# Optimization experiments

Measured on AMD Instinct MI355X. Metric: run time of the kernel, lower is better.

The kernel has to match this reference:

```python
import jax, jax.numpy as jnp
import numpy as np

NUM_BINS = 512
NUM_HEADS = 8
CHANNELS = 512
FFN_HIDDEN = 1024
BN_EPS = 1e-5


def setup_inputs() -> dict:
    key = jax.random.key(0)
    ks = jax.random.split(key, 8)
    B, C, N = 32, CHANNELS, 512
    Fh = FFN_HIDDEN
    inp = {
        "x": jax.random.normal(ks[0], (B, C, N), dtype=jnp.float32),
        "qkv_w": jax.random.normal(ks[1], (3 * C, C), dtype=jnp.float32) * 0.02,
        "qkv_b": jnp.zeros((3 * C,), jnp.float32),
        "out_w": jax.random.normal(ks[2], (C, C), dtype=jnp.float32) * 0.02,
        "out_b": jnp.zeros((C,), jnp.float32),
        "rel_pos_emb": jax.random.normal(ks[3], (2 * NUM_BINS - 1, NUM_HEADS), dtype=jnp.float32) * 0.02,
        "bn1_g": jnp.ones((C,), jnp.float32),
        "bn1_b": jnp.zeros((C,), jnp.float32),
        "bn1_m": jnp.zeros((C,), jnp.float32),
        "bn1_v": jnp.ones((C,), jnp.float32),
        "ffn1_w": jax.random.normal(ks[4], (Fh, C), dtype=jnp.float32) * 0.02,
        "ffn1_b": jnp.zeros((Fh,), jnp.float32),
        "ffn2_w": jax.random.normal(ks[5], (C, Fh), dtype=jnp.float32) * 0.02,
        "ffn2_b": jnp.zeros((C,), jnp.float32),
        "bn2_g": jnp.ones((C,), jnp.float32),
        "bn2_b": jnp.zeros((C,), jnp.float32),
        "bn2_m": jnp.zeros((C,), jnp.float32),
        "bn2_v": jnp.ones((C,), jnp.float32),
    }
    return inp


def _pw_conv(w, b, x):
    # 1x1 Conv1d == per-position linear: w [O, C], x [B, C, N] -> [B, O, N]
    return jnp.einsum('oc,bcn->bon', w, x) + b[None, :, None]


def _bn_eval(x, g, b, m, v):
    # BatchNorm1d in eval mode over channel dim of [B, C, N]
    inv = jax.lax.rsqrt(v + BN_EPS)
    return (x - m[None, :, None]) * (g * inv)[None, :, None] + b[None, :, None]


def reference(x, qkv_w, qkv_b, out_w, out_b, rel_pos_emb,
              bn1_g, bn1_b, bn1_m, bn1_v,
              ffn1_w, ffn1_b, ffn2_w, ffn2_b,
              bn2_g, bn2_b, bn2_m, bn2_v):
    B, C, N = x.shape
    H = NUM_HEADS
    Dh = C // H
    scale = Dh ** (-0.5)

    residual = x
    qkv = _pw_conv(qkv_w, qkv_b, x)                      # [B, 3C, N]
    q, k, v = jnp.split(qkv, 3, axis=1)
    # view(B, H, Dh, N).transpose(-1, -2) -> [B, H, N, Dh]
    q = jnp.swapaxes(q.reshape(B, H, Dh, N), -1, -2)
    k = jnp.swapaxes(k.reshape(B, H, Dh, N), -1, -2)
    v = jnp.swapaxes(v.reshape(B, H, Dh, N), -1, -2)

    attn = jnp.einsum('bhnd,bhmd->bhnm', q, k) * scale   # [B, H, N, N]

    # relative position bias, gathered from the table
    pos_idx = jnp.arange(N)[None, :] - jnp.arange(N)[:, None]
    pos_idx = jnp.clip(pos_idx + NUM_BINS - 1, 0, 2 * NUM_BINS - 2)
    bias = rel_pos_emb[pos_idx]                          # [N, N, H]
    attn = attn + jnp.transpose(bias, (2, 0, 1))[None]   # [1, H, N, N]

    attn = jax.nn.softmax(attn, axis=-1)
    out = jnp.einsum('bhnm,bhmd->bhnd', attn, v)         # [B, H, N, Dh]
    out = jnp.swapaxes(out, -1, -2).reshape(B, C, N)
    out = _pw_conv(out_w, out_b, out)

    h = _bn_eval(out + residual, bn1_g, bn1_b, bn1_m, bn1_v)

    f = _pw_conv(ffn1_w, ffn1_b, h)
    f = jax.nn.gelu(f, approximate=False)
    f = _pw_conv(ffn2_w, ffn2_b, f)

    return _bn_eval(f + h, bn2_g, bn2_b, bn2_m, bn2_v)
```

## Files before the change

kernel.cpp:

```cpp
#include <hip/hip_runtime.h>
#include <cstddef>
#include <cstdint>

constexpr int B_ = 32;
constexpr int C_ = 512;
constexpr int N_ = 512;
constexpr int H_ = 8;
constexpr int FH_ = 1024;
constexpr float BN_EPS_ = 1e-5f;
constexpr float LOG2E_ = 1.44269504088896f;

typedef __attribute__((ext_vector_type(8))) short bf16x8;
typedef __attribute__((ext_vector_type(4))) short s16x4;
typedef __attribute__((ext_vector_type(4))) float f32x4;

enum { EPI_QKV = 0, EPI_BN1 = 1, EPI_GELU = 2, EPI_BN2 = 3 };

__device__ inline void gload_lds16(const void* g, void* l) {
    __builtin_amdgcn_global_load_lds(
        (const __attribute__((address_space(1))) void*)g,
        (__attribute__((address_space(3))) void*)l, 16, 0, 0);
}

__device__ inline short f2bf(float f) {
    union { float f; uint32_t u; } v; v.f = f;
    uint32_t r = v.u + 0x7fffu + ((v.u >> 16) & 1u);
    return (short)(r >> 16);
}

__device__ inline float bf2f(short s) {
    union { uint32_t u; float f; } v;
    v.u = ((uint32_t)(uint16_t)s) << 16;
    return v.f;
}

__device__ inline uint32_t cvt_pk_bf16(float lo, float hi) {
    uint32_t r;
    asm("v_cvt_pk_bf16_f32 %0, %1, %2" : "=v"(r) : "v"(lo), "v"(hi));
    return r;
}

__global__ __launch_bounds__(256) void cvt_weights(
    const float* __restrict__ s0, const float* __restrict__ s1,
    const float* __restrict__ s2, const float* __restrict__ s3,
    short* __restrict__ d)
{
    int i = blockIdx.x * 256 + threadIdx.x;
    const float* src;
    int local;
    if (i < 196608)      { src = s0; local = i; }
    else if (i < 262144) { src = s1; local = i - 196608; }
    else if (i < 393216) { src = s2; local = i - 262144; }
    else                 { src = s3; local = i - 393216; }
    f32x4 v = *(const f32x4*)&src[(size_t)local * 4];
    s16x4 o;
    o[0] = f2bf(v[0]); o[1] = f2bf(v[1]); o[2] = f2bf(v[2]); o[3] = f2bf(v[3]);
    *(s16x4*)&d[(size_t)i * 4] = o;
}

__global__ __launch_bounds__(256) void transpose_x(const float* __restrict__ x,
                                                   short* __restrict__ xT)
{
    __shared__ __align__(16) float s[64][65];
    const int b = blockIdx.z, c0 = blockIdx.x * 64, n0 = blockIdx.y * 64;
    const int t = threadIdx.x;
    const float* xb = x + ((size_t)b * C_ + c0) * N_ + n0;
    {
        int nl = t & 63, cl = t >> 6;
#pragma unroll
        for (int i = 0; i < 16; ++i)
            s[cl + i * 4][nl] = xb[(size_t)(cl + i * 4) * N_ + nl];
    }
    __syncthreads();
    short* xTb = xT + ((size_t)b * N_ + n0) * C_ + c0;
    {
        int cl = t & 63, nl = t >> 6;
#pragma unroll
        for (int i = 0; i < 16; ++i)
            xTb[(size_t)(nl + i * 4) * C_ + cl] = f2bf(s[cl][nl + i * 4]);
    }
}

template <int EPI, int KD, int OSTR, int OB, int NB>
__global__ __launch_bounds__(256) void gemm_mfma(
    const short* __restrict__ A, const short* __restrict__ W,
    const float* __restrict__ bias,
    short* __restrict__ Yb, short* __restrict__ Yv, float* __restrict__ Yf,
    const short* __restrict__ resb,
    const float* __restrict__ g, const float* __restrict__ bt,
    const float* __restrict__ mn, const float* __restrict__ vr)
{
    constexpr int NWG = OB * NB * B_;
    constexpr int CPX = NWG / 8;
    const int bid = blockIdx.x;
    const int swz = (bid & 7) * CPX + (bid >> 3);
    const int ob  = swz % OB;
    const int rst = swz / OB;
    const int b   = rst / NB;
    const int o0  = ob * 128;
    const int n0  = (rst % NB) * 128;
    const short* Ab = A + (size_t)b * 512 * KD;

    __shared__ __align__(16) short As[4][128 * 32];
    __shared__ __align__(16) short Bs[4][128 * 32];

    const int t = threadIdx.x;
    const int lane = t & 63, w = t >> 6;
    const int l15 = lane & 15, lg = lane >> 4;
    const int wr = w >> 1, wc = w & 1;

    const f32x4 zero4 = {0.f, 0.f, 0.f, 0.f};
    f32x4 acc[4][4];
#pragma unroll
    for (int i = 0; i < 4; ++i)
#pragma unroll
        for (int j = 0; j < 4; ++j) acc[i][j] = zero4;

    const int r0 = t >> 2;
    const int kb = (((t & 3) ^ ((t >> 3) & 3)) * 8);

    constexpr int Kt = KD / 32;

#define GSTAGE(bufi, kk0)                                                        \
    do {                                                                         \
        gload_lds16(Ab + (size_t)(n0 + r0) * KD + (kk0) + kb,      &As[bufi][w * 512]);        \
        gload_lds16(Ab + (size_t)(n0 + r0 + 64) * KD + (kk0) + kb, &As[bufi][w * 512 + 2048]); \
        gload_lds16(W  + (size_t)(o0 + r0) * KD + (kk0) + kb,      &Bs[bufi][w * 512]);        \
        gload_lds16(W  + (size_t)(o0 + r0 + 64) * KD + (kk0) + kb, &Bs[bufi][w * 512 + 2048]); \
    } while (0)

    GSTAGE(0, 0);
    GSTAGE(1, 32);

    const int rsw = (lg ^ ((l15 >> 1) & 3)) * 8;

    for (int kt = 0; kt < Kt; kt += 4) {
#pragma unroll
        for (int u = 0; u < 4; ++u) {
            const int k = kt + u;
            if (k == Kt - 1) asm volatile("s_waitcnt vmcnt(0)" ::: "memory");
            else             asm volatile("s_waitcnt vmcnt(4)" ::: "memory");
            __builtin_amdgcn_s_barrier();
            __builtin_amdgcn_sched_barrier(0);
            if (k + 2 < Kt) GSTAGE((u + 2) & 3, (k + 2) * 32);

            bf16x8 af[4], bf[4];
#pragma unroll
            for (int mi = 0; mi < 4; ++mi)
                af[mi] = *(const bf16x8*)&As[u][(wr * 64 + mi * 16 + l15) * 32 + rsw];
#pragma unroll
            for (int ni = 0; ni < 4; ++ni)
                bf[ni] = *(const bf16x8*)&Bs[u][(wc * 64 + ni * 16 + l15) * 32 + rsw];
#pragma unroll
            for (int mi = 0; mi < 4; ++mi)
#pragma unroll
                for (int ni = 0; ni < 4; ++ni)
                    acc[mi][ni] = __builtin_amdgcn_mfma_f32_16x16x32_bf16(
                        af[mi], bf[ni], acc[mi][ni], 0, 0, 0);
        }
    }
#undef GSTAGE

#pragma unroll
    for (int mi = 0; mi < 4; ++mi) {
        const int nb2 = n0 + wr * 64 + mi * 16 + lg * 4;
#pragma unroll
        for (int ni = 0; ni < 4; ++ni) {
            const int o = o0 + wc * 64 + ni * 16 + l15;
            const float bv = bias[o];
            f32x4 v = acc[mi][ni];
            if constexpr (EPI == EPI_QKV) {
                if (o0 < 1024) {
#pragma unroll
                    for (int r = 0; r < 4; ++r)
                        Yb[((size_t)b * 512 + nb2 + r) * 1024 + o] = f2bf(v[r] + bv);
                } else {
                    s16x4 pk;
#pragma unroll
                    for (int r = 0; r < 4; ++r) pk[r] = f2bf(v[r] + bv);
                    *(s16x4*)&Yv[((size_t)b * 512 + (o - 1024)) * 512 + nb2] = pk;
                }
            } else if constexpr (EPI == EPI_BN1) {
                const float sc = g[o] * rsqrtf(vr[o] + BN_EPS_);
                const float sh = bt[o] - mn[o] * sc;
#pragma unroll
                for (int r = 0; r < 4; ++r) {
                    float rr = bf2f(resb[((size_t)b * 512 + nb2 + r) * 512 + o]);
                    float val = (v[r] + bv + rr) * sc + sh;
                    Yb[((size_t)b * 512 + nb2 + r) * 512 + o] = f2bf(val);
                }
            } else if constexpr (EPI == EPI_GELU) {
#pragma unroll
                for (int r = 0; r < 4; ++r) {
                    float val = v[r] + bv;
                    val = 0.5f * val * (1.0f + erff(val * 0.70710678118654752f));
                    Yb[((size_t)b * 512 + nb2 + r) * OSTR + o] = f2bf(val);
                }
            } else {
                const float sc = g[o] * rsqrtf(vr[o] + BN_EPS_);
                const float sh = bt[o] - mn[o] * sc;
                f32x4 ov;
#pragma unroll
                for (int r = 0; r < 4; ++r) {
                    float hres = bf2f(resb[((size_t)b * 512 + nb2 + r) * 512 + o]);
                    ov[r] = (v[r] + bv + hres) * sc + sh;
                }
                *(f32x4*)&Yf[((size_t)b * 512 + o) * 512 + nb2] = ov;
            }
        }
    }
}

__global__ __launch_bounds__(512) void attn_mfma(
    const short* __restrict__ qkT, const short* __restrict__ vT,
    const float* __restrict__ rel, short* __restrict__ attnT)
{
    const int id = blockIdx.x;
    const int h  = id & 7;
    const int n0 = ((id >> 3) & 3) * 128;
    const int b  = id >> 5;
    const int t  = threadIdx.x;
    const int lane = t & 63, w = t >> 6;
    const int l15 = lane & 15, lg = lane >> 4;

    __shared__ __align__(16) short Ks[2][64 * 64];
    __shared__ __align__(16) short Vs[2][64 * 64];
    __shared__ __align__(16) short Ps[8 * 16 * 64];
    __shared__ __align__(16) float relh[1024];

    const short* qb = qkT + (size_t)b * 512 * 1024;
    const short* vb = vT + (size_t)b * 512 * 512;

    for (int i = t; i < 1023; i += 512) relh[i] = rel[i * H_ + h] * LOG2E_;

    const int qr = w * 16 + l15;
    const short* qrow = qb + (size_t)(n0 + qr) * 1024 + h * 64;
    bf16x8 aq[2];
    aq[0] = *(const bf16x8*)&qrow[lg * 8];
    aq[1] = *(const bf16x8*)&qrow[32 + lg * 8];

#define KSTAGE(bufi, m0s)                                                        \
    do {                                                                         \
        {                                                                        \
            int fl_ = t * 8;                                                     \
            int r_ = fl_ >> 6;                                                   \
            int blk_ = (fl_ >> 3) & 7;                                           \
            int d_ = ((blk_ ^ (r_ & 7)) << 3);                                   \
            gload_lds16(qb + (size_t)((m0s) + r_) * 1024 + 512 + h * 64 + d_,    \
                        &Ks[bufi][w * 512]);                                     \
        }                                                                        \
        {                                                                        \
            int fl_ = t * 8;                                                     \
            int dr_ = fl_ >> 6;                                                  \
            int blk_ = (fl_ >> 3) & 7;                                           \
            int m_ = ((blk_ ^ (dr_ & 7)) << 3);                                  \
            gload_lds16(vb + (size_t)(h * 64 + dr_) * 512 + (m0s) + m_,          \
                        &Vs[bufi][w * 512]);                                     \
        }                                                                        \
    } while (0)

    KSTAGE(0, 0);
    __syncthreads();

    const f32x4 zero4 = {0.f, 0.f, 0.f, 0.f};
    f32x4 acc_o[4];
#pragma unroll
    for (int dj = 0; dj < 4; ++dj) acc_o[dj] = zero4;

    float rmax = -3e38f, rsum = 0.f;

    const int qglob = n0 + qr;

    int cur = 0;
    for (int tile = 0; tile < 8; ++tile) {
        const int m0 = tile * 64;
        if (tile < 7) KSTAGE(cur ^ 1, m0 + 64);

        f32x4 s4[4];
#pragma unroll
        for (int mi = 0; mi < 4; ++mi) s4[mi] = zero4;
#pragma unroll
        for (int kk = 0; kk < 2; ++kk) {
#pragma unroll
            for (int mi = 0; mi < 4; ++mi) {
                int mr = mi * 16 + l15;
                bf16x8 bk = *(const bf16x8*)&Ks[cur][mr * 64 + (((kk * 4 + lg) ^ (mr & 7)) << 3)];
                s4[mi] = __builtin_amdgcn_mfma_f32_16x16x32_bf16(bk, aq[kk], s4[mi], 0, 0, 0);
            }
        }

        const int ib = m0 + lg * 4 - qglob + 511;
        float tmax = -3e38f;
#pragma unroll
        for (int mi = 0; mi < 4; ++mi)
#pragma unroll
            for (int r = 0; r < 4; ++r) {
                float sv = s4[mi][r] * (0.125f * LOG2E_) + relh[ib + mi * 16 + r];
                s4[mi][r] = sv;
                tmax = fmaxf(tmax, sv);
            }
        tmax = fmaxf(tmax, __shfl_xor(tmax, 16));
        tmax = fmaxf(tmax, __shfl_xor(tmax, 32));

        if (!__all(tmax <= rmax + 8.f)) {
            float nm = fmaxf(rmax, tmax);
            float sc = __builtin_amdgcn_exp2f(rmax - nm);
            rmax = nm;
            rsum *= sc;
            float scl[4];
#pragma unroll
            for (int r = 0; r < 4; ++r)
                scl[r] = __shfl(sc, (lane & 48) | (lg * 4 + r));
#pragma unroll
            for (int dj = 0; dj < 4; ++dj)
#pragma unroll
                for (int r = 0; r < 4; ++r) acc_o[dj][r] *= scl[r];
        }

        float ts = 0.f;
#pragma unroll
        for (int mi = 0; mi < 4; ++mi)
#pragma unroll
            for (int r = 0; r < 4; ++r) {
                float p = __builtin_amdgcn_exp2f(s4[mi][r] - rmax);
                s4[mi][r] = p;
                ts += p;
            }
        ts += __shfl_xor(ts, 16);
        ts += __shfl_xor(ts, 32);
        rsum += ts;

#pragma unroll
        for (int mi = 0; mi < 4; ++mi) {
            uint32_t w01 = cvt_pk_bf16(s4[mi][0], s4[mi][1]);
            uint32_t w23 = cvt_pk_bf16(s4[mi][2], s4[mi][3]);
            int blk = mi * 2 + (lg >> 1);
            int idx = w * 1024 + l15 * 64 + ((blk ^ (l15 & 7)) << 3) + ((lg & 1) << 2);
            *(uint2*)&Ps[idx] = make_uint2(w01, w23);
        }

#pragma unroll
        for (int kk = 0; kk < 2; ++kk) {
            bf16x8 ap = *(const bf16x8*)&Ps[w * 1024 + l15 * 64 + (((kk * 4 + lg) ^ (l15 & 7)) << 3)];
#pragma unroll
            for (int dj = 0; dj < 4; ++dj) {
                int dr = dj * 16 + l15;
                bf16x8 bv = *(const bf16x8*)&Vs[cur][dr * 64 + (((kk * 4 + lg) ^ (dr & 7)) << 3)];
                acc_o[dj] = __builtin_amdgcn_mfma_f32_16x16x32_bf16(ap, bv, acc_o[dj], 0, 0, 0);
            }
        }
        __syncthreads();
        cur ^= 1;
    }
#undef KSTAGE

    float inv = 1.f / rsum;
    float invr[4];
#pragma unroll
    for (int r = 0; r < 4; ++r)
        invr[r] = __shfl(inv, (lane & 48) | (lg * 4 + r));

    short* ob = attnT + (size_t)b * 512 * 512;
#pragma unroll
    for (int dj = 0; dj < 4; ++dj)
#pragma unroll
        for (int reg = 0; reg < 4; ++reg) {
            int nglob = n0 + w * 16 + lg * 4 + reg;
            ob[(size_t)nglob * 512 + h * 64 + dj * 16 + l15] =
                f2bf(acc_o[dj][reg] * invr[reg]);
        }
}

extern "C" void kernel_launch(void* const* d_in, const int* in_sizes, int n_in,
                              void* d_out, int out_size, void* d_ws, size_t ws_size,
                              hipStream_t stream)
{
    const float* x      = (const float*)d_in[0];
    const float* qkv_w  = (const float*)d_in[1];
    const float* qkv_b  = (const float*)d_in[2];
    const float* out_w  = (const float*)d_in[3];
    const float* out_b  = (const float*)d_in[4];
    const float* rel    = (const float*)d_in[5];
    const float* bn1_g  = (const float*)d_in[6];
    const float* bn1_b  = (const float*)d_in[7];
    const float* bn1_m  = (const float*)d_in[8];
    const float* bn1_v  = (const float*)d_in[9];
    const float* ffn1_w = (const float*)d_in[10];
    const float* ffn1_b = (const float*)d_in[11];
    const float* ffn2_w = (const float*)d_in[12];
    const float* ffn2_b = (const float*)d_in[13];
    const float* bn2_g  = (const float*)d_in[14];
    const float* bn2_b  = (const float*)d_in[15];
    const float* bn2_m  = (const float*)d_in[16];
    const float* bn2_v  = (const float*)d_in[17];

    float* out = (float*)d_out;
    short* ws  = (short*)d_ws;

    size_t off = 0;
    short* qkvw_bf = ws + off; off += (size_t)1536 * 512;
    short* outw_bf = ws + off; off += (size_t)512 * 512;
    short* f1w_bf  = ws + off; off += (size_t)1024 * 512;
    short* f2w_bf  = ws + off; off += (size_t)512 * 1024;
    short* xT      = ws + off; off += (size_t)B_ * 512 * 512;
    short* qkT     = ws + off; off += (size_t)B_ * 512 * 1024;
    short* vTb     = ws + off; off += (size_t)B_ * 512 * 512;
    short* attnT   = ws + off; off += (size_t)B_ * 512 * 512;
    short* h_bf    = ws + off; off += (size_t)B_ * 512 * 512;
    short* f1_bf   = ws + off; off += (size_t)B_ * 512 * 1024;

    const dim3 blk(256);

    cvt_weights<<<dim3(524288 / 256), blk, 0, stream>>>(qkv_w, out_w, ffn1_w, ffn2_w, qkvw_bf);

    transpose_x<<<dim3(8, 8, B_), blk, 0, stream>>>(x, xT);

    gemm_mfma<EPI_QKV, 512, 1024, 12, 4><<<dim3(1536), blk, 0, stream>>>(
        xT, qkvw_bf, qkv_b, qkT, vTb, nullptr, nullptr, nullptr, nullptr, nullptr, nullptr);

    attn_mfma<<<dim3(1024), dim3(512), 0, stream>>>(qkT, vTb, rel, attnT);

    gemm_mfma<EPI_BN1, 512, 512, 4, 4><<<dim3(512), blk, 0, stream>>>(
        attnT, outw_bf, out_b, h_bf, nullptr, nullptr, xT, bn1_g, bn1_b, bn1_m, bn1_v);

    gemm_mfma<EPI_GELU, 512, 1024, 8, 4><<<dim3(1024), blk, 0, stream>>>(
        h_bf, f1w_bf, ffn1_b, f1_bf, nullptr, nullptr, nullptr, nullptr, nullptr, nullptr, nullptr);

    gemm_mfma<EPI_BN2, 1024, 512, 4, 4><<<dim3(512), blk, 0, stream>>>(
        f1_bf, f2w_bf, ffn2_b, nullptr, nullptr, out, h_bf, bn2_g, bn2_b, bn2_m, bn2_v);
}
```

Before: 170.8 us.

## Enlarge GEMM tiles to 256x128 with 512-thread blocks and triple buffering

The GEMM kernel now uses 512-thread workgroups (8 waves) covering a 256-row by 128-output tile, so each weight tile loaded into LDS is reused across twice as many positions. The LDS ring drops from four to three stages so the larger A tile still fits, and the wait counts and stage indexing are adjusted to match. Grid sizes are halved for all four GEMMs. This cuts redundant weight traffic and the number of workgroups, but gives fewer blocks per GPU, a shallower prefetch ring, and possibly lower occupancy.

Measured after the change: 183.2 us. 7.3% more time.

```diff
diff --git a/kernel.cpp b/kernel.cpp
--- a/kernel.cpp
+++ b/kernel.cpp
@@ -81,8 +81,8 @@
     }
 }
 
-template <int EPI, int KD, int OSTR, int OB, int NB>
-__global__ __launch_bounds__(256) void gemm_mfma(
+template <int EPI, int KD, int OSTR, int OB>
+__global__ __launch_bounds__(512) void gemm_mfma(
     const short* __restrict__ A, const short* __restrict__ W,
     const float* __restrict__ bias,
     short* __restrict__ Yb, short* __restrict__ Yv, float* __restrict__ Yf,
@@ -90,6 +90,7 @@
     const float* __restrict__ g, const float* __restrict__ bt,
     const float* __restrict__ mn, const float* __restrict__ vr)
 {
+    constexpr int NB = 2;
     constexpr int NWG = OB * NB * B_;
     constexpr int CPX = NWG / 8;
     const int bid = blockIdx.x;
@@ -98,16 +99,16 @@
     const int rst = swz / OB;
     const int b   = rst / NB;
     const int o0  = ob * 128;
-    const int n0  = (rst % NB) * 128;
+    const int n0  = (rst % NB) * 256;
     const short* Ab = A + (size_t)b * 512 * KD;
 
-    __shared__ __align__(16) short As[4][128 * 32];
-    __shared__ __align__(16) short Bs[4][128 * 32];
+    __shared__ __align__(16) short As[3][256 * 32];
+    __shared__ __align__(16) short Bs[3][128 * 32];
 
     const int t = threadIdx.x;
     const int lane = t & 63, w = t >> 6;
     const int l15 = lane & 15, lg = lane >> 4;
-    const int wr = w >> 1, wc = w & 1;
+    const int wn = w >> 1, wo = w & 1;
 
     const f32x4 zero4 = {0.f, 0.f, 0.f, 0.f};
     f32x4 acc[4][4];
@@ -123,10 +124,9 @@
 
 #define GSTAGE(bufi, kk0)                                                        \
     do {                                                                         \
-        gload_lds16(Ab + (size_t)(n0 + r0) * KD + (kk0) + kb,      &As[bufi][w * 512]);        \
-        gload_lds16(Ab + (size_t)(n0 + r0 + 64) * KD + (kk0) + kb, &As[bufi][w * 512 + 2048]); \
-        gload_lds16(W  + (size_t)(o0 + r0) * KD + (kk0) + kb,      &Bs[bufi][w * 512]);        \
-        gload_lds16(W  + (size_t)(o0 + r0 + 64) * KD + (kk0) + kb, &Bs[bufi][w * 512 + 2048]); \
+        gload_lds16(Ab + (size_t)(n0 + r0) * KD + (kk0) + kb,       &As[bufi][w * 512]);        \
+        gload_lds16(Ab + (size_t)(n0 + r0 + 128) * KD + (kk0) + kb, &As[bufi][4096 + w * 512]); \
+        gload_lds16(W  + (size_t)(o0 + r0) * KD + (kk0) + kb,       &Bs[bufi][w * 512]);        \
     } while (0)
 
     GSTAGE(0, 0);
@@ -134,39 +134,41 @@
 
     const int rsw = (lg ^ ((l15 >> 1) & 3)) * 8;
 
-    for (int kt = 0; kt < Kt; kt += 4) {
-#pragma unroll
-        for (int u = 0; u < 4; ++u) {
+    for (int kt = 0; kt < Kt; kt += 3) {
+#pragma unroll
+        for (int u = 0; u < 3; ++u) {
             const int k = kt + u;
-            if (k == Kt - 1) asm volatile("s_waitcnt vmcnt(0)" ::: "memory");
-            else             asm volatile("s_waitcnt vmcnt(4)" ::: "memory");
-            __builtin_amdgcn_s_barrier();
-            __builtin_amdgcn_sched_barrier(0);
-            if (k + 2 < Kt) GSTAGE((u + 2) & 3, (k + 2) * 32);
-
-            bf16x8 af[4], bf[4];
-#pragma unroll
-            for (int mi = 0; mi < 4; ++mi)
-                af[mi] = *(const bf16x8*)&As[u][(wr * 64 + mi * 16 + l15) * 32 + rsw];
-#pragma unroll
-            for (int ni = 0; ni < 4; ++ni)
-                bf[ni] = *(const bf16x8*)&Bs[u][(wc * 64 + ni * 16 + l15) * 32 + rsw];
-#pragma unroll
-            for (int mi = 0; mi < 4; ++mi)
+            if (k < Kt) {
+                if (k == Kt - 1) asm volatile("s_waitcnt vmcnt(0)" ::: "memory");
+                else             asm volatile("s_waitcnt vmcnt(3)" ::: "memory");
+                __builtin_amdgcn_s_barrier();
+                __builtin_amdgcn_sched_barrier(0);
+                if (k + 2 < Kt) GSTAGE((u + 2) % 3, (k + 2) * 32);
+
+                bf16x8 af[4], bf[4];
+#pragma unroll
+                for (int mi = 0; mi < 4; ++mi)
+                    af[mi] = *(const bf16x8*)&As[u][(wn * 64 + mi * 16 + l15) * 32 + rsw];
 #pragma unroll
                 for (int ni = 0; ni < 4; ++ni)
-                    acc[mi][ni] = __builtin_amdgcn_mfma_f32_16x16x32_bf16(
-                        af[mi], bf[ni], acc[mi][ni], 0, 0, 0);
+                    bf[ni] = *(const bf16x8*)&Bs[u][(wo * 64 + ni * 16 + l15) * 32 + rsw];
+#pragma unroll
+                for (int mi = 0; mi < 4; ++mi)
+#pragma unroll
+                    for (int ni = 0; ni < 4; ++ni)
+                        acc[mi][ni] = __builtin_amdgcn_mfma_f32_16x16x32_bf16(
+                            af[mi], bf[ni], acc[mi][ni], 0, 0, 0);
+            }
         }
     }
 #undef GSTAGE
 
 #pragma unroll
     for (int mi = 0; mi < 4; ++mi) {
-        const int nb2 = n0 + wr * 64 + mi * 16 + lg * 4;
+        const int nb2 = n0 + wn * 64 + mi * 16 + lg * 4;
 #pragma unroll
         for (int ni = 0; ni < 4; ++ni) {
-            const int o = o0 + wc * 64 + ni * 16 + l15;
+            const int o = o0 + wo * 64 + ni * 16 + l15;
             const float bv = bias[o];
             f32x4 v = acc[mi][ni];
             if constexpr (EPI == EPI_QKV) {
@@ -268,7 +270,6 @@
     for (int dj = 0; dj < 4; ++dj) acc_o[dj] = zero4;
 
     float rmax = -3e38f, rsum = 0.f;
-
     const int qglob = n0 + qr;
 
     int cur = 0;
@@ -410,22 +411,23 @@
     short* f1_bf   = ws + off; off += (size_t)B_ * 512 * 1024;
 
     const dim3 blk(256);
+    const dim3 blk512(512);
 
     cvt_weights<<<dim3(524288 / 256), blk, 0, stream>>>(qkv_w, out_w, ffn1_w, ffn2_w, qkvw_bf);
 
     transpose_x<<<dim3(8, 8, B_), blk, 0, stream>>>(x, xT);
 
-    gemm_mfma<EPI_QKV, 512, 1024, 12, 4><<<dim3(1536), blk, 0, stream>>>(
+    gemm_mfma<EPI_QKV, 512, 1024, 12><<<dim3(768), blk512, 0, stream>>>(
         xT, qkvw_bf, qkv_b, qkT, vTb, nullptr, nullptr, nullptr, nullptr, nullptr, nullptr);
 
-    attn_mfma<<<dim3(1024), dim3(512), 0, stream>>>(qkT, vTb, rel, attnT);
-
-    gemm_mfma<EPI_BN1, 512, 512, 4, 4><<<dim3(512), blk, 0, stream>>>(
+    attn_mfma<<<dim3(1024), blk512, 0, stream>>>(qkT, vTb, rel, attnT);
+
+    gemm_mfma<EPI_BN1, 512, 512, 4><<<dim3(256), blk512, 0, stream>>>(
         attnT, outw_bf, out_b, h_bf, nullptr, nullptr, xT, bn1_g, bn1_b, bn1_m, bn1_v);
 
-    gemm_mfma<EPI_GELU, 512, 1024, 8, 4><<<dim3(1024), blk, 0, stream>>>(
+    gemm_mfma<EPI_GELU, 512, 1024, 8><<<dim3(512), blk512, 0, stream>>>(
         h_bf, f1w_bf, ffn1_b, f1_bf, nullptr, nullptr, nullptr, nullptr, nullptr, nullptr, nullptr);
 
-    gemm_mfma<EPI_BN2, 1024, 512, 4, 4><<<dim3(512), blk, 0, stream>>>(
+    gemm_mfma<EPI_BN2, 1024, 512, 4><<<dim3(256), blk512, 0, stream>>>(
         f1_bf, f2w_bf, ffn2_b, nullptr, nullptr, out, h_bf, bn2_g, bn2_b, bn2_m, bn2_v);
 }
```
